# Kernel tuning notes

Hardware: AMD Instinct MI355X
Metric: run time of the kernel (lower is better)

The kernel has to match this reference:

```python
import jax, jax.numpy as jnp
import numpy as np

B, IMG, D, HEADS, L, PC, PF, OUT = 8, 128, 128, 4, 2, 8, 4, 32
HC = IMG // PC; NC = HC * HC          # 16x16 -> 256 coarse tokens
HF = IMG // PF; NF = HF * HF          # 32x32 -> 1024 fine tokens


def _ln(x, g, b):
    m = x.mean(-1, keepdims=True)
    v = x.var(-1, keepdims=True)
    return (x - m) * jax.lax.rsqrt(v + 1e-5) * g + b


def _conv(x, w, b, pad):
    y = jax.lax.conv_general_dilated(x, w, (1, 1), ((pad, pad), (pad, pad)),
                                     dimension_numbers=('NCHW', 'OIHW', 'NCHW'))
    return y + b[None, :, None, None]


def _bilinear_ac(x, oh, ow):  # F.interpolate(mode='bilinear', align_corners=True)
    _, _, H, W = x.shape
    ys = jnp.linspace(0.0, H - 1.0, oh)
    xs = jnp.linspace(0.0, W - 1.0, ow)
    y0 = jnp.floor(ys).astype(jnp.int32); y1 = jnp.minimum(y0 + 1, H - 1); wy = (ys - y0)[:, None]
    x0 = jnp.floor(xs).astype(jnp.int32); x1 = jnp.minimum(x0 + 1, W - 1); wx = (xs - x0)[None, :]
    g = lambda yi, xi: x[:, :, yi][:, :, :, xi]
    return (g(y0, x0) * (1 - wy) * (1 - wx) + g(y0, x1) * (1 - wy) * wx
            + g(y1, x0) * wy * (1 - wx) + g(y1, x1) * wy * wx)


def _patchify(x, p):  # F.unfold with kernel=stride=p, in_chans=1
    b, _, h, w = x.shape
    return x.reshape(b, h // p, p, w // p, p).transpose(0, 1, 3, 2, 4).reshape(b, (h // p) * (w // p), p * p)


def _forward(x, Wpc, bpc, Wpf, bpf, type_embed, ln1_g, ln1_b, Wqkv, Wo, bo,
             ln2_g, ln2_b, W1, b1, W2, b2, dWc, dbc, dWf, dbf, fW1, fb1, fW2, fb2):
    Bx = x.shape[0]
    # ---- multi-scale patch embed ----
    coarse = _patchify(x, PC) @ Wpc + bpc + type_embed[0]   # [B,NC,D]
    fine = _patchify(x, PF) @ Wpf + bpf                     # [B,NF,D]
    # ---- edge map: sobel -> avgpool(4) -> threshold at per-image mean ----
    gray = x.mean(1, keepdims=True)
    kx = jnp.array([[[[-1, 0, 1], [-2, 0, 2], [-1, 0, 1]]]], x.dtype)
    ky = jnp.array([[[[-1, -2, -1], [0, 0, 0], [1, 2, 1]]]], x.dtype)
    sx = _conv(gray, kx, jnp.zeros((1,), x.dtype), 1)
    sy = _conv(gray, ky, jnp.zeros((1,), x.dtype), 1)
    e = jnp.sqrt(sx ** 2 + sy ** 2)
    e = e.reshape(Bx, 1, IMG // 4, 4, IMG // 4, 4).mean((3, 5))  # [B,1,32,32] == fine grid
    mask_flat = (e > e.mean((2, 3), keepdims=True)).reshape(Bx, NF)
    # ---- static-shape analogue of per-sample masked gather + pad_sequence:
    # stable sort puts edge tokens first (original pixel order preserved), pads are zeros
    order = jnp.argsort(jnp.logical_not(mask_flat), axis=1, stable=True)   # [B,NF]
    mask_sorted = jnp.take_along_axis(mask_flat, order, 1)
    fine_sorted = jnp.take_along_axis(fine, order[..., None], 1) * mask_sorted[..., None]
    fine_sorted = fine_sorted + type_embed[1]   # type embed added to pads too (as in torch)
    tokens = jnp.concatenate([coarse, fine_sorted], axis=1)   # [B,N,D]
    N = NC + NF
    hd = D // HEADS
    scale = hd ** -0.5
    # ---- encoder blocks (pre-LN attn + MLP, irregular-token path) ----
    for l in range(L):
        y = _ln(tokens, ln1_g[l], ln1_b[l])
        qkv = (y @ Wqkv[l]).reshape(Bx, N, 3, HEADS, hd).transpose(2, 0, 3, 1, 4)
        q, k, v = qkv[0], qkv[1], qkv[2]
        attn = jax.nn.softmax(jnp.einsum('bhqd,bhkd->bhqk', q, k) * scale, axis=-1)
        o = jnp.einsum('bhqk,bhkd->bhqd', attn, v).transpose(0, 2, 1, 3).reshape(Bx, N, D)
        tokens = tokens + o @ Wo[l] + bo[l]
        y = _ln(tokens, ln2_g[l], ln2_b[l])
        tokens = tokens + jax.nn.gelu(y @ W1[l] + b1[l], approximate=False) @ W2[l] + b2[l]
    # ---- multi-scale decoder ----
    c = (tokens[:, :NC] @ dWc + dbc).reshape(Bx, HC, HC, 1).transpose(0, 3, 1, 2)
    c_up = _bilinear_ac(c, OUT, OUT)
    feats = (tokens[:, NC:] @ dWf + dbf) * mask_sorted[..., None]   # pads stay zero
    inv = jnp.argsort(order, axis=1)                                # scatter back to pixel order
    f_flat = jnp.take_along_axis(feats, inv[..., None], 1)          # [B,NF,1]
    f_map = f_flat.reshape(Bx, HF, HF, 1).transpose(0, 3, 1, 2)
    f_up = _bilinear_ac(f_map, OUT, OUT)
    fused = jnp.concatenate([c_up, f_up], axis=1)
    h = jax.nn.relu(_conv(fused, fW1, fb1, 1))
    return _conv(h, fW2, fb2, 1)   # [B,1,32,32]


def setup_inputs() -> dict:
    key = jax.random.key(0)
    ks = jax.random.split(key, 16)
    n = lambda k, shape: jax.random.normal(k, shape, jnp.float32) * 0.02
    z = lambda *shape: jnp.zeros(shape, jnp.float32)
    return {
        'x': jax.random.normal(ks[0], (B, 1, IMG, IMG), jnp.float32),
        'Wpc': n(ks[1], (PC * PC, D)), 'bpc': z(D),
        'Wpf': n(ks[2], (PF * PF, D)), 'bpf': z(D),
        'type_embed': n(ks[3], (2, D)),
        'ln1_g': jnp.ones((L, D), jnp.float32), 'ln1_b': z(L, D),
        'Wqkv': n(ks[4], (L, D, 3 * D)),
        'Wo': n(ks[5], (L, D, D)), 'bo': z(L, D),
        'ln2_g': jnp.ones((L, D), jnp.float32), 'ln2_b': z(L, D),
        'W1': n(ks[6], (L, D, 2 * D)), 'b1': z(L, 2 * D),
        'W2': n(ks[7], (L, 2 * D, D)), 'b2': z(L, D),
        'dWc': n(ks[8], (D, 1)), 'dbc': z(1),
        'dWf': n(ks[9], (D, 1)), 'dbf': z(1),
        'fW1': n(ks[10], (2, 2, 3, 3)) * 10.0, 'fb1': z(2),
        'fW2': n(ks[11], (1, 2, 3, 3)) * 10.0, 'fb2': z(1),
    }


def reference(x, Wpc, bpc, Wpf, bpf, type_embed, ln1_g, ln1_b, Wqkv, Wo, bo,
              ln2_g, ln2_b, W1, b1, W2, b2, dWc, dbc, dWf, dbf, fW1, fb1, fW2, fb2):
    return _forward(x, Wpc, bpc, Wpf, bpf, type_embed, ln1_g, ln1_b, Wqkv, Wo, bo,
                    ln2_g, ln2_b, W1, b1, W2, b2, dWc, dbc, dWf, dbf, fW1, fb1, fW2, fb2)
```

## Files before the change

kernel.cpp:

```cpp
#include <hip/hip_runtime.h>
#include <math.h>

#define Bx 8
#define IMG 128
#define DD 128
#define HEADS 4
#define LL 2
#define PCc 8
#define PFf 4
#define HCc 16
#define NCc 256
#define HFf 32
#define NFf 1024
#define NTOK 1280
#define HD 32
#define SPLIT 4
#define NQT 20

typedef __attribute__((ext_vector_type(8))) short short8;
typedef __attribute__((ext_vector_type(4))) float f32x4;

__device__ __forceinline__ short f2bf(float f) {
  unsigned u = __builtin_bit_cast(unsigned, f);
  u += 0x7FFF + ((u >> 16) & 1);
  return (short)(u >> 16);
}
__device__ __forceinline__ float bf2f(short s) {
  unsigned u = ((unsigned)(unsigned short)s) << 16;
  return __builtin_bit_cast(float, u);
}

__global__ __launch_bounds__(256) void k_prologue(const float* __restrict__ x,
    const float* __restrict__ Wpc, const float* __restrict__ bpc,
    const float* __restrict__ Wpf, const float* __restrict__ bpf,
    const float* __restrict__ te,
    const float* __restrict__ Wqkv, const float* __restrict__ Wo,
    const float* __restrict__ W1, const float* __restrict__ W2,
    short* __restrict__ WtQKV, short* __restrict__ WtO,
    short* __restrict__ Wt1, short* __restrict__ Wt2,
    float* __restrict__ e, float* __restrict__ tokens,
    float* __restrict__ fineb) {
  int blk = blockIdx.x;
  int t = threadIdx.x;
  if (blk < 1024) {
    int idx = blk * 256 + t;
    int l = idx / 131072, r = idx % 131072;
    const float* src; short* dst; int N, off;
    if (r < 49152)      { src = Wqkv + l * 49152; dst = WtQKV + l * 49152; N = 384; off = r; }
    else if (r < 65536) { src = Wo + l * 16384;  dst = WtO + l * 16384;  N = 128; off = r - 49152; }
    else if (r < 98304) { src = W1 + l * 32768;  dst = Wt1 + l * 32768;  N = 256; off = r - 65536; }
    else                { src = W2 + l * 32768;  dst = Wt2 + l * 32768;  N = 128; off = r - 98304; }
    int k = off / N, n = off % N;
    int K = (r >= 98304) ? 256 : 128;
    dst[(size_t)n * K + k] = f2bf(src[off]);
  } else if (blk < 1536) {
    int bt = blk - 1024;
    int b = bt >> 6, tile = bt & 63;
    int ty = tile >> 3, tx = tile & 7;
    int ly = t >> 4, lx = t & 15;
    int py = ty * 16 + ly, px = tx * 16 + lx;
    const float* img = x + (size_t)b * IMG * IMG;
    float v[3][3];
    #pragma unroll
    for (int ky = 0; ky < 3; ++ky)
      #pragma unroll
      for (int kx = 0; kx < 3; ++kx) {
        int yy = py + ky - 1, xx = px + kx - 1;
        v[ky][kx] = (yy >= 0 && yy < IMG && xx >= 0 && xx < IMG)
                        ? img[yy * IMG + xx] : 0.f;
      }
    float gx = -v[0][0] + v[0][2] - 2.f * v[1][0] + 2.f * v[1][2] - v[2][0] + v[2][2];
    float gy = -v[0][0] - 2.f * v[0][1] - v[0][2] + v[2][0] + 2.f * v[2][1] + v[2][2];
    __shared__ float sm[256];
    sm[t] = sqrtf(gx * gx + gy * gy);
    __syncthreads();
    if (t < 16) {
      int cy = t >> 2, cx = t & 3;
      float s = 0.f;
      #pragma unroll
      for (int dy = 0; dy < 4; ++dy)
        #pragma unroll
        for (int dx = 0; dx < 4; ++dx) s += sm[(cy * 4 + dy) * 16 + cx * 4 + dx];
      e[b * NFf + (ty * 4 + cy) * 32 + tx * 4 + cx] = s * (1.f / 16.f);
    }
  } else if (blk < 2560) {
    int bt = (blk - 1536) * 2 + (t >> 7);
    int b = bt / NCc, tok = bt % NCc;
    int hc = tok / HCc, wc = tok % HCc;
    int half = t >> 7, d = t & 127;
    __shared__ float patch[2][PCc * PCc];
    if (d < PCc * PCc) {
      int pi = d / PCc, pj = d % PCc;
      patch[half][d] = x[(b * IMG + hc * PCc + pi) * IMG + wc * PCc + pj];
    }
    __syncthreads();
    float acc = bpc[d] + te[d];
    #pragma unroll 8
    for (int i = 0; i < PCc * PCc; ++i) acc += patch[half][i] * Wpc[i * DD + d];
    tokens[(size_t)(b * NTOK + tok) * DD + d] = acc;
  } else {
    int ft = (blk - 2560) * 2 + (t >> 7);
    int b = ft >> 10, tloc = ft & 1023;
    int hf = tloc >> 5, wf = tloc & 31;
    int half = t >> 7, d = t & 127;
    __shared__ float patch[2][PFf * PFf];
    if (d < PFf * PFf) {
      int pi = d / PFf, pj = d % PFf;
      patch[half][d] = x[(b * IMG + hf * PFf + pi) * IMG + wf * PFf + pj];
    }
    __syncthreads();
    float acc = bpf[d];
    #pragma unroll
    for (int i = 0; i < PFf * PFf; ++i) acc += patch[half][i] * Wpf[i * DD + d];
    fineb[(size_t)(b * NFf + tloc) * DD + d] = acc;
  }
}

__global__ __launch_bounds__(1024) void k_edge_sort(const float* __restrict__ e,
    int* __restrict__ order, float* __restrict__ msort) {
  int b = blockIdx.x;
  int t = threadIdx.x;
  int lane = t & 63, wave = t >> 6;
  float ev = e[b * NFf + t];
  __shared__ float wsum[16];
  __shared__ int wcnt[16];
  float r = ev;
  #pragma unroll
  for (int o = 32; o > 0; o >>= 1) r += __shfl_xor(r, o, 64);
  if (lane == 0) wsum[wave] = r;
  __syncthreads();
  float tot = 0.f;
  #pragma unroll
  for (int i = 0; i < 16; ++i) tot += wsum[i];
  float mean = tot * (1.f / 1024.f);
  int m = (ev > mean) ? 1 : 0;
  unsigned long long bal = __ballot(m);
  if (lane == 0) wcnt[wave] = __popcll(bal);
  __syncthreads();
  int wbase = 0, total = 0;
  #pragma unroll
  for (int i = 0; i < 16; ++i) {
    int c = wcnt[i];
    if (i < wave) wbase += c;
    total += c;
  }
  unsigned long long below = (lane == 63) ? ~0ULL : ((1ULL << (lane + 1)) - 1);
  int incl = __popcll(bal & below);
  int eb = wbase + incl - m;
  int pos = m ? eb : (total + t - eb);
  order[b * NFf + pos] = t;
  msort[b * NFf + pos] = (float)m;
}

__global__ __launch_bounds__(256) void k_gather_ln(float* __restrict__ tokens,
    const float* __restrict__ fineb, const int* __restrict__ order,
    const float* __restrict__ msort, const float* __restrict__ te,
    const float* __restrict__ g, const float* __restrict__ bb,
    short* __restrict__ outp) {
  int row = blockIdx.x * 4 + (threadIdx.x >> 6);
  int lane = threadIdx.x & 63;
  int b = row / NTOK, r = row % NTOK;
  float2 v;
  if (r < NCc) {
    v = ((const float2*)(tokens + (size_t)row * DD))[lane];
  } else {
    int pos = r - NCc;
    int src = order[b * NFf + pos];
    float mk = msort[b * NFf + pos];
    float2 u = ((const float2*)(fineb + (size_t)(b * NFf + src) * DD))[lane];
    float2 tv = ((const float2*)(te + DD))[lane];
    v.x = u.x * mk + tv.x;
    v.y = u.y * mk + tv.y;
    ((float2*)(tokens + (size_t)row * DD))[lane] = v;
  }
  float s = v.x + v.y;
  #pragma unroll
  for (int o = 32; o > 0; o >>= 1) s += __shfl_xor(s, o, 64);
  float mean = s * (1.f / 128.f);
  float cx = v.x - mean, cy = v.y - mean;
  float q = cx * cx + cy * cy;
  #pragma unroll
  for (int o = 32; o > 0; o >>= 1) q += __shfl_xor(q, o, 64);
  float rstd = rsqrtf(q * (1.f / 128.f) + 1e-5f);
  float2 gg = ((const float2*)g)[lane];
  float2 bv = ((const float2*)bb)[lane];
  int p = (int)(unsigned short)f2bf(cx * rstd * gg.x + bv.x)
        | ((int)(unsigned short)f2bf(cy * rstd * gg.y + bv.y) << 16);
  ((int*)(outp + (size_t)row * DD))[lane] = p;
}

__global__ __launch_bounds__(256) void k_gemm_mfma(const short* __restrict__ A,
    const short* __restrict__ Wt, const float* __restrict__ bias,
    float* __restrict__ Cf, short* __restrict__ Cb, int K, int N, int do_gelu) {
  __shared__ short Alds[64 * 128];
  __shared__ short Blds[64 * 128];
  int row0 = blockIdx.x * 64, col0 = blockIdx.y * 64;
  int t = threadIdx.x;
  int lane = t & 63, w = t >> 6;
  int m = lane & 15, quad = lane >> 4;
  int lrow = lane >> 4, jphys = lane & 15;
  f32x4 zero = {0.f, 0.f, 0.f, 0.f};
  f32x4 acc[4] = {zero, zero, zero, zero};

  for (int kb = 0; kb < K; kb += 128) {
    __syncthreads();
    #pragma unroll
    for (int j = 0; j < 4; ++j) {
      int c = j * 4 + w;
      int r = c * 4 + lrow;
      int jlog = jphys ^ (r & 15);
      __builtin_amdgcn_global_load_lds(
          (const unsigned*)&A[(size_t)(row0 + r) * K + kb + jlog * 8],
          (unsigned*)&Alds[c * 512], 16, 0, 0);
      __builtin_amdgcn_global_load_lds(
          (const unsigned*)&Wt[(size_t)(col0 + r) * K + kb + jlog * 8],
          (unsigned*)&Blds[c * 512], 16, 0, 0);
    }
    __syncthreads();
    #pragma unroll
    for (int ks = 0; ks < 4; ++ks) {
      int pc = ((quad + ks * 4) ^ m) * 8;
      short8 af = *(const short8*)&Alds[(w * 16 + m) * 128 + pc];
      #pragma unroll
      for (int nt = 0; nt < 4; ++nt) {
        short8 bf = *(const short8*)&Blds[(nt * 16 + m) * 128 + pc];
        acc[nt] = __builtin_amdgcn_mfma_f32_16x16x32_bf16(af, bf, acc[nt], 0, 0, 0);
      }
    }
  }
  #pragma unroll
  for (int nt = 0; nt < 4; ++nt) {
    int col = col0 + nt * 16 + m;
    float bv = bias ? bias[col] : 0.f;
    #pragma unroll
    for (int r = 0; r < 4; ++r) {
      int row = row0 + w * 16 + quad * 4 + r;
      float v = acc[nt][r] + bv;
      if (do_gelu) v = 0.5f * v * (1.f + erff(v * 0.70710678118654752f));
      if (Cf) Cf[(size_t)row * N + col] += v;
      else    Cb[(size_t)row * N + col] = f2bf(v);
    }
  }
}

__global__ __launch_bounds__(256) void k_fused(const short* __restrict__ Opart,
    const float* __restrict__ Lpart, const short* __restrict__ WtO,
    const float* __restrict__ bo_, const float* __restrict__ ln2g_,
    const float* __restrict__ ln2b_, const short* __restrict__ Wt1,
    const float* __restrict__ b1_, const short* __restrict__ Wt2,
    const float* __restrict__ b2_, float* __restrict__ tokens,
    const float* __restrict__ ln1g_, const float* __restrict__ ln1b_,
    const short* __restrict__ WtQ, short* __restrict__ qkvb) {
  __shared__ short Blds[128 * 128];
  __shared__ short AH[32 * 268];
  __shared__ short Ylds[32 * 136];
  __shared__ float pls[2][32], plq[2][32];
  int row0 = blockIdx.x * 32;
  int b = row0 / NTOK;
  int rloc = row0 % NTOK;
  int qt = rloc >> 6, qoff = rloc & 63;
  int t = threadIdx.x;
  int lane = t & 63, w = t >> 6;
  int m = lane & 15, quad = lane >> 4;
  int rt = w >> 1, ch = w & 1;
  int lrow = lane >> 4, jphys = lane & 15;
  f32x4 zero = {0.f, 0.f, 0.f, 0.f};

  #pragma unroll
  for (int j = 0; j < 8; ++j) {
    int c = j * 4 + w;
    int r = c * 4 + lrow;
    int jlog = jphys ^ (r & 15);
    __builtin_amdgcn_global_load_lds(
        (const unsigned*)&WtO[(size_t)r * 128 + jlog * 8],
        (unsigned*)&Blds[c * 512], 16, 0, 0);
  }
  #pragma unroll
  for (int it = 0; it < 2; ++it) {
    int idx = t + it * 256;
    int q = idx >> 4, j = idx & 15;
    int dh = j >> 2, dd = (j & 3) * 8;
    int qg = qoff + q;
    size_t pb = ((size_t)(b * HEADS + dh) * NQT + qt) * SPLIT;
    float L = Lpart[(pb + 0) * 64 + qg] + Lpart[(pb + 1) * 64 + qg]
            + Lpart[(pb + 2) * 64 + qg] + Lpart[(pb + 3) * 64 + qg];
    float o[8] = {0, 0, 0, 0, 0, 0, 0, 0};
    #pragma unroll
    for (int sk = 0; sk < SPLIT; ++sk) {
      short8 po = *(const short8*)&Opart[(pb + sk) * 2048 + qg * 32 + dd];
      #pragma unroll
      for (int i = 0; i < 8; ++i) o[i] += bf2f(po[i]);
    }
    float rs = 1.f / L;
    short8 ov;
    #pragma unroll
    for (int i = 0; i < 8; ++i) ov[i] = f2bf(o[i] * rs);
    *(short8*)&AH[q * 136 + j * 8] = ov;
  }
  __syncthreads();
  f32x4 acc[4] = {zero, zero, zero, zero};
  #pragma unroll
  for (int ks = 0; ks < 4; ++ks) {
    short8 af = *(const short8*)&AH[(rt * 16 + m) * 136 + quad * 8 + ks * 32];
    int pc = ((quad + ks * 4) ^ m) * 8;
    #pragma unroll
    for (int nt = 0; nt < 4; ++nt) {
      short8 bf = *(const short8*)&Blds[(ch * 64 + nt * 16 + m) * 128 + pc];
      acc[nt] = __builtin_amdgcn_mfma_f32_16x16x32_bf16(af, bf, acc[nt], 0, 0, 0);
    }
  }
  float v[4][4];
  #pragma unroll
  for (int nt = 0; nt < 4; ++nt) {
    int col = ch * 64 + nt * 16 + m;
    float bv = bo_[col];
    #pragma unroll
    for (int r = 0; r < 4; ++r) {
      int row = row0 + rt * 16 + quad * 4 + r;
      v[nt][r] = acc[nt][r] + bv + tokens[(size_t)row * DD + col];
    }
  }
  #pragma unroll
  for (int r = 0; r < 4; ++r) {
    float s = v[0][r] + v[1][r] + v[2][r] + v[3][r];
    float q = v[0][r] * v[0][r] + v[1][r] * v[1][r]
            + v[2][r] * v[2][r] + v[3][r] * v[3][r];
    #pragma unroll
    for (int o = 1; o < 16; o <<= 1) { s += __shfl_xor(s, o); q += __shfl_xor(q, o); }
    if (m == 0) {
      int lr = rt * 16 + quad * 4 + r;
      pls[ch][lr] = s;
      plq[ch][lr] = q;
    }
  }
  __syncthreads();
  #pragma unroll
  for (int r = 0; r < 4; ++r) {
    int lr = rt * 16 + quad * 4 + r;
    float S = pls[0][lr] + pls[1][lr];
    float Q = plq[0][lr] + plq[1][lr];
    float mean = S * (1.f / 128.f);
    float var = Q * (1.f / 128.f) - mean * mean;
    float rstd = rsqrtf(var + 1e-5f);
    #pragma unroll
    for (int nt = 0; nt < 4; ++nt) {
      int col = ch * 64 + nt * 16 + m;
      Ylds[lr * 136 + col] = f2bf((v[nt][r] - mean) * rstd * ln2g_[col] + ln2b_[col]);
    }
  }
  for (int hh = 0; hh < 2; ++hh) {
    #pragma unroll
    for (int j = 0; j < 8; ++j) {
      int c = j * 4 + w;
      int r = c * 4 + lrow;
      int jlog = jphys ^ (r & 15);
      __builtin_amdgcn_global_load_lds(
          (const unsigned*)&Wt1[(size_t)(hh * 128 + r) * 128 + jlog * 8],
          (unsigned*)&Blds[c * 512], 16, 0, 0);
    }
    __syncthreads();
    f32x4 ha[4] = {zero, zero, zero, zero};
    #pragma unroll
    for (int ks = 0; ks < 4; ++ks) {
      short8 af = *(const short8*)&Ylds[(rt * 16 + m) * 136 + quad * 8 + ks * 32];
      int pc = ((quad + ks * 4) ^ m) * 8;
      #pragma unroll
      for (int nt = 0; nt < 4; ++nt) {
        short8 bf = *(const short8*)&Blds[(ch * 64 + nt * 16 + m) * 128 + pc];
        ha[nt] = __builtin_amdgcn_mfma_f32_16x16x32_bf16(af, bf, ha[nt], 0, 0, 0);
      }
    }
    #pragma unroll
    for (int nt = 0; nt < 4; ++nt) {
      int n = hh * 128 + ch * 64 + nt * 16 + m;
      float bv = b1_[n];
      #pragma unroll
      for (int r = 0; r < 4; ++r) {
        float vv = ha[nt][r] + bv;
        vv = 0.5f * vv * (1.f + erff(vv * 0.70710678118654752f));
        AH[(rt * 16 + quad * 4 + r) * 268 + n] = f2bf(vv);
      }
    }
    __syncthreads();
  }
  f32x4 a2[4] = {zero, zero, zero, zero};
  for (int kb = 0; kb < 2; ++kb) {
    if (kb) __syncthreads();
    #pragma unroll
    for (int j = 0; j < 8; ++j) {
      int c = j * 4 + w;
      int r = c * 4 + lrow;
      int jlog = jphys ^ (r & 15);
      __builtin_amdgcn_global_load_lds(
          (const unsigned*)&Wt2[(size_t)r * 256 + kb * 128 + jlog * 8],
          (unsigned*)&Blds[c * 512], 16, 0, 0);
    }
    __syncthreads();
    #pragma unroll
    for (int ks = 0; ks < 4; ++ks) {
      int pc = ((quad + ks * 4) ^ m) * 8;
      short8 af = *(const short8*)&AH[(rt * 16 + m) * 268 + kb * 128
                                      + quad * 8 + ks * 32];
      #pragma unroll
      for (int nt = 0; nt < 4; ++nt) {
        short8 bf = *(const short8*)&Blds[(ch * 64 + nt * 16 + m) * 128 + pc];
        a2[nt] = __builtin_amdgcn_mfma_f32_16x16x32_bf16(af, bf, a2[nt], 0, 0, 0);
      }
    }
  }
  #pragma unroll
  for (int nt = 0; nt < 4; ++nt) {
    int col = ch * 64 + nt * 16 + m;
    float bv = b2_[col];
    #pragma unroll
    for (int r = 0; r < 4; ++r) {
      int row = row0 + rt * 16 + quad * 4 + r;
      float val = a2[nt][r] + bv + v[nt][r];
      tokens[(size_t)row * DD + col] = val;
      v[nt][r] = val;
    }
  }
  if (ln1g_ == nullptr) return;
  #pragma unroll
  for (int r = 0; r < 4; ++r) {
    float s = v[0][r] + v[1][r] + v[2][r] + v[3][r];
    float q = v[0][r] * v[0][r] + v[1][r] * v[1][r]
            + v[2][r] * v[2][r] + v[3][r] * v[3][r];
    #pragma unroll
    for (int o = 1; o < 16; o <<= 1) { s += __shfl_xor(s, o); q += __shfl_xor(q, o); }
    if (m == 0) {
      int lr = rt * 16 + quad * 4 + r;
      pls[ch][lr] = s;
      plq[ch][lr] = q;
    }
  }
  __syncthreads();
  #pragma unroll
  for (int r = 0; r < 4; ++r) {
    int lr = rt * 16 + quad * 4 + r;
    float S = pls[0][lr] + pls[1][lr];
    float Q = plq[0][lr] + plq[1][lr];
    float mean = S * (1.f / 128.f);
    float var = Q * (1.f / 128.f) - mean * mean;
    float rstd = rsqrtf(var + 1e-5f);
    #pragma unroll
    for (int nt = 0; nt < 4; ++nt) {
      int col = ch * 64 + nt * 16 + m;
      Ylds[lr * 136 + col] = f2bf((v[nt][r] - mean) * rstd * ln1g_[col] + ln1b_[col]);
    }
  }
  for (int c3 = 0; c3 < 3; ++c3) {
    if (c3) __syncthreads();
    #pragma unroll
    for (int j = 0; j < 8; ++j) {
      int c = j * 4 + w;
      int r = c * 4 + lrow;
      int jlog = jphys ^ (r & 15);
      __builtin_amdgcn_global_load_lds(
          (const unsigned*)&WtQ[(size_t)(c3 * 128 + r) * 128 + jlog * 8],
          (unsigned*)&Blds[c * 512], 16, 0, 0);
    }
    __syncthreads();
    f32x4 qa[4] = {zero, zero, zero, zero};
    #pragma unroll
    for (int ks = 0; ks < 4; ++ks) {
      short8 af = *(const short8*)&Ylds[(rt * 16 + m) * 136 + quad * 8 + ks * 32];
      int pc = ((quad + ks * 4) ^ m) * 8;
      #pragma unroll
      for (int nt = 0; nt < 4; ++nt) {
        short8 bf = *(const short8*)&Blds[(ch * 64 + nt * 16 + m) * 128 + pc];
        qa[nt] = __builtin_amdgcn_mfma_f32_16x16x32_bf16(af, bf, qa[nt], 0, 0, 0);
      }
    }
    #pragma unroll
    for (int nt = 0; nt < 4; ++nt) {
      int col = c3 * 128 + ch * 64 + nt * 16 + m;
      #pragma unroll
      for (int r = 0; r < 4; ++r) {
        int row = row0 + rt * 16 + quad * 4 + r;
        qkvb[(size_t)row * 384 + col] = f2bf(qa[nt][r]);
      }
    }
  }
}

__global__ __launch_bounds__(256) void k_attn4(const short* __restrict__ qkv,
    short* __restrict__ Opart, float* __restrict__ Lpart) {
  __shared__ short Ks[64 * 32];
  __shared__ short Vt[32 * 74];
  __shared__ short Pl[4][16 * 74];

  int sk = blockIdx.x % SPLIT;
  int qt = (blockIdx.x / SPLIT) % NQT;
  int h  = (blockIdx.x / (SPLIT * NQT)) % HEADS;
  int b  = blockIdx.x / (SPLIT * NQT * HEADS);
  int t = threadIdx.x;
  int lane = t & 63, w = t >> 6;
  int m = lane & 15, quad = lane >> 4;
  int q0 = qt * 64 + w * 16;

  const float scale = 0.17677669529663687f;
  short8 qraw = *(const short8*)(qkv + ((size_t)(b * NTOK) + q0 + m) * 384 + h * HD + quad * 8);
  short8 qf;
  #pragma unroll
  for (int j = 0; j < 8; ++j) qf[j] = f2bf(bf2f(qraw[j]) * scale);

  f32x4 zero = {0.f, 0.f, 0.f, 0.f};
  f32x4 Oacc[2] = {zero, zero};
  float psum[4] = {0.f, 0.f, 0.f, 0.f};

  int skey = t >> 2, sdseg = t & 3;
  int jlogK = sdseg ^ ((skey >> 1) & 3);
  const short* kstage = qkv + ((size_t)(b * NTOK) + skey) * 384 + 128 + h * HD + jlogK * 8;
  const short* vstage = qkv + ((size_t)(b * NTOK) + skey) * 384 + 256 + h * HD + sdseg * 8;
  int kswz = (quad ^ ((m >> 1) & 3)) * 8;

  for (int s = sk * 5; s < sk * 5 + 5; ++s) {
    __syncthreads();
    __builtin_amdgcn_global_load_lds((const unsigned*)(kstage + (size_t)s * 64 * 384),
                                     (unsigned*)&Ks[w * 512], 16, 0, 0);
    short8 vf = *(const short8*)(vstage + (size_t)s * 64 * 384);
    #pragma unroll
    for (int j = 0; j < 8; ++j) Vt[(sdseg * 8 + j) * 74 + skey] = vf[j];
    __syncthreads();

    f32x4 sc[4];
    #pragma unroll
    for (int ct = 0; ct < 4; ++ct) {
      short8 kfrag = *(const short8*)&Ks[(ct * 16 + m) * 32 + kswz];
      sc[ct] = __builtin_amdgcn_mfma_f32_16x16x32_bf16(qf, kfrag, zero, 0, 0, 0);
    }
    #pragma unroll
    for (int ct = 0; ct < 4; ++ct)
      #pragma unroll
      for (int r = 0; r < 4; ++r) {
        float p = __expf(sc[ct][r]);
        unsigned u = __builtin_bit_cast(unsigned, p);
        psum[r] += __builtin_bit_cast(float, u & 0xffff0000u);
        Pl[w][(quad * 4 + r) * 74 + ct * 16 + m] = (short)(u >> 16);
      }
    #pragma unroll
    for (int ks = 0; ks < 2; ++ks) {
      short8 pfrag = *(const short8*)&Pl[w][m * 74 + ks * 32 + quad * 8];
      #pragma unroll
      for (int nt = 0; nt < 2; ++nt) {
        short8 vfrag = *(const short8*)&Vt[(nt * 16 + m) * 74 + ks * 32 + quad * 8];
        Oacc[nt] = __builtin_amdgcn_mfma_f32_16x16x32_bf16(pfrag, vfrag, Oacc[nt], 0, 0, 0);
      }
    }
  }
  #pragma unroll
  for (int r = 0; r < 4; ++r) {
    float ssum = psum[r];
    #pragma unroll
    for (int o = 1; o < 16; o <<= 1) ssum += __shfl_xor(ssum, o);
    int qloc = w * 16 + quad * 4 + r;
    #pragma unroll
    for (int nt = 0; nt < 2; ++nt)
      Opart[(size_t)blockIdx.x * 2048 + qloc * 32 + nt * 16 + m] = f2bf(Oacc[nt][r]);
    if (m == 0) Lpart[(size_t)blockIdx.x * 64 + qloc] = ssum;
  }
}

__global__ __launch_bounds__(1024) void k_decoder(const float* __restrict__ tokens,
    const float* __restrict__ dWc, const float* __restrict__ dbc,
    const float* __restrict__ dWf, const float* __restrict__ dbf,
    const float* __restrict__ msort, const int* __restrict__ order,
    const float* __restrict__ fW1, const float* __restrict__ fb1,
    const float* __restrict__ fW2, const float* __restrict__ fb2,
    float* __restrict__ outp) {
  int b = blockIdx.x;
  int t = threadIdx.x;
  __shared__ float cmap[NCc];
  __shared__ float fmap[1024];
  __shared__ float cup[1024];
  __shared__ float hb[2][1024];
  {
    const float* row = tokens + (size_t)(b * NTOK + NCc + t) * DD;
    float a = 0.f;
    #pragma unroll 8
    for (int d4 = 0; d4 < 32; ++d4) {
      float4 u = ((const float4*)row)[d4];
      float4 wv = ((const float4*)dWf)[d4];
      a += u.x * wv.x + u.y * wv.y + u.z * wv.z + u.w * wv.w;
    }
    a = (a + dbf[0]) * msort[b * NFf + t];
    fmap[order[b * NFf + t]] = a;
  }
  if (t < NCc) {
    const float* row = tokens + (size_t)(b * NTOK + t) * DD;
    float a = 0.f;
    #pragma unroll 8
    for (int d4 = 0; d4 < 32; ++d4) {
      float4 u = ((const float4*)row)[d4];
      float4 wv = ((const float4*)dWc)[d4];
      a += u.x * wv.x + u.y * wv.y + u.z * wv.z + u.w * wv.w;
    }
    cmap[t] = a + dbc[0];
  }
  __syncthreads();
  int y = t >> 5, x = t & 31;
  {
    float ys = y * (15.f / 31.f);
    float xs = x * (15.f / 31.f);
    int y0 = (int)floorf(ys); int y1 = min(y0 + 1, 15); float wy = ys - (float)y0;
    int x0 = (int)floorf(xs); int x1 = min(x0 + 1, 15); float wx = xs - (float)x0;
    cup[t] = cmap[y0 * 16 + x0] * (1.f - wy) * (1.f - wx)
           + cmap[y0 * 16 + x1] * (1.f - wy) * wx
           + cmap[y1 * 16 + x0] * wy * (1.f - wx)
           + cmap[y1 * 16 + x1] * wy * wx;
  }
  __syncthreads();
  for (int oc = 0; oc < 2; ++oc) {
    float a = fb1[oc];
    #pragma unroll
    for (int ic = 0; ic < 2; ++ic)
      #pragma unroll
      for (int ky = 0; ky < 3; ++ky)
        #pragma unroll
        for (int kx = 0; kx < 3; ++kx) {
          int yy = y + ky - 1, xx = x + kx - 1;
          float v = 0.f;
          if (yy >= 0 && yy < 32 && xx >= 0 && xx < 32)
            v = ic == 0 ? cup[yy * 32 + xx] : fmap[yy * 32 + xx];
          a += v * fW1[((oc * 2 + ic) * 3 + ky) * 3 + kx];
        }
    hb[oc][t] = fmaxf(a, 0.f);
  }
  __syncthreads();
  float a = fb2[0];
  #pragma unroll
  for (int ic = 0; ic < 2; ++ic)
    #pragma unroll
    for (int ky = 0; ky < 3; ++ky)
      #pragma unroll
      for (int kx = 0; kx < 3; ++kx) {
        int yy = y + ky - 1, xx = x + kx - 1;
        float v = (yy >= 0 && yy < 32 && xx >= 0 && xx < 32)
                      ? hb[ic][yy * 32 + xx] : 0.f;
        a += v * fW2[(ic * 3 + ky) * 3 + kx];
      }
  outp[b * 1024 + t] = a;
}

extern "C" void kernel_launch(void* const* d_in, const int* in_sizes, int n_in,
                              void* d_out, int out_size, void* d_ws, size_t ws_size,
                              hipStream_t stream) {
  const float* x    = (const float*)d_in[0];
  const float* Wpc  = (const float*)d_in[1];
  const float* bpc  = (const float*)d_in[2];
  const float* Wpf  = (const float*)d_in[3];
  const float* bpf  = (const float*)d_in[4];
  const float* te   = (const float*)d_in[5];
  const float* ln1g = (const float*)d_in[6];
  const float* ln1b = (const float*)d_in[7];
  const float* Wqkv = (const float*)d_in[8];
  const float* Wo   = (const float*)d_in[9];
  const float* bo   = (const float*)d_in[10];
  const float* ln2g = (const float*)d_in[11];
  const float* ln2b = (const float*)d_in[12];
  const float* W1   = (const float*)d_in[13];
  const float* b1   = (const float*)d_in[14];
  const float* W2   = (const float*)d_in[15];
  const float* b2   = (const float*)d_in[16];
  const float* dWc  = (const float*)d_in[17];
  const float* dbc  = (const float*)d_in[18];
  const float* dWf  = (const float*)d_in[19];
  const float* dbf  = (const float*)d_in[20];
  const float* fW1  = (const float*)d_in[21];
  const float* fb1  = (const float*)d_in[22];
  const float* fW2  = (const float*)d_in[23];
  const float* fb2  = (const float*)d_in[24];

  char* ws = (char*)d_ws;
  float* tokens = (float*)ws;                 ws += 1310720 * 4;
  float* fineb  = (float*)ws;                 ws += 1048576 * 4;
  short* ybuf   = (short*)ws;                 ws += 1310720 * 2;
  short* qkvb   = (short*)ws;                 ws += 3932160 * 2;
  short* Opart  = (short*)ws;                 ws += (size_t)(Bx * HEADS * NQT * SPLIT) * 2048 * 2;
  float* Lpart  = (float*)ws;                 ws += (size_t)(Bx * HEADS * NQT * SPLIT) * 64 * 4;
  short* WtQKV  = (short*)ws;                 ws += 98304 * 2;
  short* WtO    = (short*)ws;                 ws += 32768 * 2;
  short* Wt1    = (short*)ws;                 ws += 65536 * 2;
  short* Wt2    = (short*)ws;                 ws += 65536 * 2;
  float* ebuf   = (float*)ws;                 ws += 8192 * 4;
  float* msort  = (float*)ws;                 ws += 8192 * 4;
  int*   order  = (int*)ws;                   ws += 8192 * 4;

  const int M = Bx * NTOK;

  k_prologue<<<6656, 256, 0, stream>>>(x, Wpc, bpc, Wpf, bpf, te, Wqkv, Wo, W1, W2,
                                       WtQKV, WtO, Wt1, Wt2, ebuf, tokens, fineb);
  k_edge_sort<<<Bx, 1024, 0, stream>>>(ebuf, order, msort);
  k_gather_ln<<<M / 4, 256, 0, stream>>>(tokens, fineb, order, msort, te,
                                         ln1g, ln1b, ybuf);

  k_gemm_mfma<<<dim3(M / 64, 384 / 64), 256, 0, stream>>>(
      ybuf, WtQKV, nullptr, nullptr, qkvb, 128, 384, 0);
  k_attn4<<<Bx * HEADS * NQT * SPLIT, 256, 0, stream>>>(qkvb, Opart, Lpart);
  k_fused<<<M / 32, 256, 0, stream>>>(
      Opart, Lpart, WtO, bo, ln2g, ln2b,
      Wt1, b1, Wt2, b2, tokens,
      ln1g + DD, ln1b + DD, WtQKV + 49152, qkvb);

  k_attn4<<<Bx * HEADS * NQT * SPLIT, 256, 0, stream>>>(qkvb, Opart, Lpart);
  k_fused<<<M / 32, 256, 0, stream>>>(
      Opart, Lpart, WtO + 16384, bo + DD, ln2g + DD, ln2b + DD,
      Wt1 + 32768, b1 + 256, Wt2 + 32768, b2 + DD, tokens,
      nullptr, nullptr, nullptr, nullptr);

  k_decoder<<<Bx, 1024, 0, stream>>>(tokens, dWc, dbc, dWf, dbf, msort, order,
                                     fW1, fb1, fW2, fb2, (float*)d_out);
}
```

Measured before the change: 236.1 us.

## Fuse gather+LN1 with QKV GEMM and move decoder projection into last fused kernel

Merges the gather/LayerNorm kernel and the separate QKV GEMM into a single kernel that normalizes 32 rows into LDS and multiplies them by the QKV weight. This removes the bf16 ybuf round trip and one launch. The final fused layer now computes the per-token decoder dot products (dWc/dWf) from registers and writes a small hrow buffer, so the decoder no longer rereads the full token tensor. It also issues weight tile loads earlier so they overlap the LayerNorm math. The trade-off is extra sync points and larger LDS use in the gather kernel.

```diff
diff --git a/kernel.cpp b/kernel.cpp
--- a/kernel.cpp
+++ b/kernel.cpp
@@ -152,93 +152,96 @@
   msort[b * NFf + pos] = (float)m;
 }
 
-__global__ __launch_bounds__(256) void k_gather_ln(float* __restrict__ tokens,
+__global__ __launch_bounds__(256) void k_gather_qkv(float* __restrict__ tokens,
     const float* __restrict__ fineb, const int* __restrict__ order,
     const float* __restrict__ msort, const float* __restrict__ te,
     const float* __restrict__ g, const float* __restrict__ bb,
-    short* __restrict__ outp) {
-  int row = blockIdx.x * 4 + (threadIdx.x >> 6);
-  int lane = threadIdx.x & 63;
-  int b = row / NTOK, r = row % NTOK;
-  float2 v;
-  if (r < NCc) {
-    v = ((const float2*)(tokens + (size_t)row * DD))[lane];
-  } else {
-    int pos = r - NCc;
-    int src = order[b * NFf + pos];
-    float mk = msort[b * NFf + pos];
-    float2 u = ((const float2*)(fineb + (size_t)(b * NFf + src) * DD))[lane];
-    float2 tv = ((const float2*)(te + DD))[lane];
-    v.x = u.x * mk + tv.x;
-    v.y = u.y * mk + tv.y;
-    ((float2*)(tokens + (size_t)row * DD))[lane] = v;
-  }
-  float s = v.x + v.y;
-  #pragma unroll
-  for (int o = 32; o > 0; o >>= 1) s += __shfl_xor(s, o, 64);
-  float mean = s * (1.f / 128.f);
-  float cx = v.x - mean, cy = v.y - mean;
-  float q = cx * cx + cy * cy;
-  #pragma unroll
-  for (int o = 32; o > 0; o >>= 1) q += __shfl_xor(q, o, 64);
-  float rstd = rsqrtf(q * (1.f / 128.f) + 1e-5f);
-  float2 gg = ((const float2*)g)[lane];
-  float2 bv = ((const float2*)bb)[lane];
-  int p = (int)(unsigned short)f2bf(cx * rstd * gg.x + bv.x)
-        | ((int)(unsigned short)f2bf(cy * rstd * gg.y + bv.y) << 16);
-  ((int*)(outp + (size_t)row * DD))[lane] = p;
-}
-
-__global__ __launch_bounds__(256) void k_gemm_mfma(const short* __restrict__ A,
-    const short* __restrict__ Wt, const float* __restrict__ bias,
-    float* __restrict__ Cf, short* __restrict__ Cb, int K, int N, int do_gelu) {
-  __shared__ short Alds[64 * 128];
-  __shared__ short Blds[64 * 128];
-  int row0 = blockIdx.x * 64, col0 = blockIdx.y * 64;
+    const short* __restrict__ WtQ, short* __restrict__ qkvb) {
+  __shared__ short Blds[128 * 128];
+  __shared__ short Ylds[32 * 136];
+  int row0 = blockIdx.x * 32;
   int t = threadIdx.x;
   int lane = t & 63, w = t >> 6;
   int m = lane & 15, quad = lane >> 4;
+  int rt = w >> 1, ch = w & 1;
   int lrow = lane >> 4, jphys = lane & 15;
   f32x4 zero = {0.f, 0.f, 0.f, 0.f};
-  f32x4 acc[4] = {zero, zero, zero, zero};
-
-  for (int kb = 0; kb < K; kb += 128) {
-    __syncthreads();
-    #pragma unroll
-    for (int j = 0; j < 4; ++j) {
-      int c = j * 4 + w;
-      int r = c * 4 + lrow;
-      int jlog = jphys ^ (r & 15);
-      __builtin_amdgcn_global_load_lds(
-          (const unsigned*)&A[(size_t)(row0 + r) * K + kb + jlog * 8],
-          (unsigned*)&Alds[c * 512], 16, 0, 0);
-      __builtin_amdgcn_global_load_lds(
-          (const unsigned*)&Wt[(size_t)(col0 + r) * K + kb + jlog * 8],
-          (unsigned*)&Blds[c * 512], 16, 0, 0);
-    }
-    __syncthreads();
+
+  #pragma unroll
+  for (int j = 0; j < 8; ++j) {
+    int c = j * 4 + w;
+    int r = c * 4 + lrow;
+    int jlog = jphys ^ (r & 15);
+    __builtin_amdgcn_global_load_lds(
+        (const unsigned*)&WtQ[(size_t)r * 128 + jlog * 8],
+        (unsigned*)&Blds[c * 512], 16, 0, 0);
+  }
+  float2 gg = ((const float2*)g)[lane];
+  float2 bv = ((const float2*)bb)[lane];
+  #pragma unroll
+  for (int rr = 0; rr < 8; ++rr) {
+    int lr = w * 8 + rr;
+    int row = row0 + lr;
+    int b = row / NTOK, rl = row % NTOK;
+    float2 v;
+    if (rl < NCc) {
+      v = ((const float2*)(tokens + (size_t)row * DD))[lane];
+    } else {
+      int pos = rl - NCc;
+      int src = order[b * NFf + pos];
+      float mk = msort[b * NFf + pos];
+      float2 u = ((const float2*)(fineb + (size_t)(b * NFf + src) * DD))[lane];
+      float2 tv = ((const float2*)(te + DD))[lane];
+      v.x = u.x * mk + tv.x;
+      v.y = u.y * mk + tv.y;
+      ((float2*)(tokens + (size_t)row * DD))[lane] = v;
+    }
+    float s = v.x + v.y;
+    #pragma unroll
+    for (int o = 32; o > 0; o >>= 1) s += __shfl_xor(s, o, 64);
+    float mean = s * (1.f / 128.f);
+    float cx = v.x - mean, cy = v.y - mean;
+    float q = cx * cx + cy * cy;
+    #pragma unroll
+    for (int o = 32; o > 0; o >>= 1) q += __shfl_xor(q, o, 64);
+    float rstd = rsqrtf(q * (1.f / 128.f) + 1e-5f);
+    int p = (int)(unsigned short)f2bf(cx * rstd * gg.x + bv.x)
+          | ((int)(unsigned short)f2bf(cy * rstd * gg.y + bv.y) << 16);
+    ((int*)Ylds)[lr * 68 + lane] = p;
+  }
+  for (int c3 = 0; c3 < 3; ++c3) {
+    if (c3) {
+      __syncthreads();
+      #pragma unroll
+      for (int j = 0; j < 8; ++j) {
+        int c = j * 4 + w;
+        int r = c * 4 + lrow;
+        int jlog = jphys ^ (r & 15);
+        __builtin_amdgcn_global_load_lds(
+            (const unsigned*)&WtQ[(size_t)(c3 * 128 + r) * 128 + jlog * 8],
+            (unsigned*)&Blds[c * 512], 16, 0, 0);
+      }
+    }
+    __syncthreads();
+    f32x4 qa[4] = {zero, zero, zero, zero};
     #pragma unroll
     for (int ks = 0; ks < 4; ++ks) {
+      short8 af = *(const short8*)&Ylds[(rt * 16 + m) * 136 + quad * 8 + ks * 32];
       int pc = ((quad + ks * 4) ^ m) * 8;
-      short8 af = *(const short8*)&Alds[(w * 16 + m) * 128 + pc];
       #pragma unroll
       for (int nt = 0; nt < 4; ++nt) {
-        short8 bf = *(const short8*)&Blds[(nt * 16 + m) * 128 + pc];
-        acc[nt] = __builtin_amdgcn_mfma_f32_16x16x32_bf16(af, bf, acc[nt], 0, 0, 0);
-      }
-    }
-  }
-  #pragma unroll
-  for (int nt = 0; nt < 4; ++nt) {
-    int col = col0 + nt * 16 + m;
-    float bv = bias ? bias[col] : 0.f;
-    #pragma unroll
-    for (int r = 0; r < 4; ++r) {
-      int row = row0 + w * 16 + quad * 4 + r;
-      float v = acc[nt][r] + bv;
-      if (do_gelu) v = 0.5f * v * (1.f + erff(v * 0.70710678118654752f));
-      if (Cf) Cf[(size_t)row * N + col] += v;
-      else    Cb[(size_t)row * N + col] = f2bf(v);
+        short8 bf = *(const short8*)&Blds[(ch * 64 + nt * 16 + m) * 128 + pc];
+        qa[nt] = __builtin_amdgcn_mfma_f32_16x16x32_bf16(af, bf, qa[nt], 0, 0, 0);
+      }
+    }
+    #pragma unroll
+    for (int nt = 0; nt < 4; ++nt) {
+      int col = c3 * 128 + ch * 64 + nt * 16 + m;
+      #pragma unroll
+      for (int r = 0; r < 4; ++r) {
+        int row = row0 + rt * 16 + quad * 4 + r;
+        qkvb[(size_t)row * 384 + col] = f2bf(qa[nt][r]);
+      }
     }
   }
 }
@@ -250,7 +253,10 @@
     const float* __restrict__ b1_, const short* __restrict__ Wt2,
     const float* __restrict__ b2_, float* __restrict__ tokens,
     const float* __restrict__ ln1g_, const float* __restrict__ ln1b_,
-    const short* __restrict__ WtQ, short* __restrict__ qkvb) {
+    const short* __restrict__ WtQ, short* __restrict__ qkvb,
+    const float* __restrict__ dWc_, const float* __restrict__ dbc_,
+    const float* __restrict__ dWf_, const float* __restrict__ dbf_,
+    float* __restrict__ hrow) {
   __shared__ short Blds[128 * 128];
   __shared__ short AH[32 * 268];
   __shared__ short Ylds[32 * 136];
@@ -335,6 +341,15 @@
   }
   __syncthreads();
   #pragma unroll
+  for (int j = 0; j < 8; ++j) {
+    int c = j * 4 + w;
+    int r = c * 4 + lrow;
+    int jlog = jphys ^ (r & 15);
+    __builtin_amdgcn_global_load_lds(
+        (const unsigned*)&Wt1[(size_t)r * 128 + jlog * 8],
+        (unsigned*)&Blds[c * 512], 16, 0, 0);
+  }
+  #pragma unroll
   for (int r = 0; r < 4; ++r) {
     int lr = rt * 16 + quad * 4 + r;
     float S = pls[0][lr] + pls[1][lr];
@@ -349,14 +364,17 @@
     }
   }
   for (int hh = 0; hh < 2; ++hh) {
-    #pragma unroll
-    for (int j = 0; j < 8; ++j) {
-      int c = j * 4 + w;
-      int r = c * 4 + lrow;
-      int jlog = jphys ^ (r & 15);
-      __builtin_amdgcn_global_load_lds(
-          (const unsigned*)&Wt1[(size_t)(hh * 128 + r) * 128 + jlog * 8],
-          (unsigned*)&Blds[c * 512], 16, 0, 0);
+    if (hh) {
+      __syncthreads();
+      #pragma unroll
+      for (int j = 0; j < 8; ++j) {
+        int c = j * 4 + w;
+        int r = c * 4 + lrow;
+        int jlog = jphys ^ (r & 15);
+        __builtin_amdgcn_global_load_lds(
+            (const unsigned*)&Wt1[(size_t)(128 + r) * 128 + jlog * 8],
+            (unsigned*)&Blds[c * 512], 16, 0, 0);
+      }
     }
     __syncthreads();
     f32x4 ha[4] = {zero, zero, zero, zero};
@@ -381,11 +399,10 @@
         AH[(rt * 16 + quad * 4 + r) * 268 + n] = f2bf(vv);
       }
     }
-    __syncthreads();
   }
   f32x4 a2[4] = {zero, zero, zero, zero};
   for (int kb = 0; kb < 2; ++kb) {
-    if (kb) __syncthreads();
+    __syncthreads();
     #pragma unroll
     for (int j = 0; j < 8; ++j) {
       int c = j * 4 + w;
@@ -420,7 +437,31 @@
       v[nt][r] = val;
     }
   }
-  if (ln1g_ == nullptr) return;
+  if (ln1g_ == nullptr) {
+    bool coarse = (rloc < NCc);
+    const float* dw = coarse ? dWc_ : dWf_;
+    float dwv[4];
+    #pragma unroll
+    for (int nt = 0; nt < 4; ++nt) dwv[nt] = dw[ch * 64 + nt * 16 + m];
+    #pragma unroll
+    for (int r = 0; r < 4; ++r) {
+      float s = v[0][r] * dwv[0] + v[1][r] * dwv[1]
+              + v[2][r] * dwv[2] + v[3][r] * dwv[3];
+      #pragma unroll
+      for (int o = 1; o < 16; o <<= 1) s += __shfl_xor(s, o);
+      if (m == 0) pls[ch][rt * 16 + quad * 4 + r] = s;
+    }
+    __syncthreads();
+    if (m == 0 && ch == 0) {
+      float dbv = coarse ? dbc_[0] : dbf_[0];
+      #pragma unroll
+      for (int r = 0; r < 4; ++r) {
+        int lr = rt * 16 + quad * 4 + r;
+        hrow[row0 + lr] = pls[0][lr] + pls[1][lr] + dbv;
+      }
+    }
+    return;
+  }
   #pragma unroll
   for (int r = 0; r < 4; ++r) {
     float s = v[0][r] + v[1][r] + v[2][r] + v[3][r];
@@ -435,6 +476,15 @@
     }
   }
   __syncthreads();
+  #pragma unroll
+  for (int j = 0; j < 8; ++j) {
+    int c = j * 4 + w;
+    int r = c * 4 + lrow;
+    int jlog = jphys ^ (r & 15);
+    __builtin_amdgcn_global_load_lds(
+        (const unsigned*)&WtQ[(size_t)r * 128 + jlog * 8],
+        (unsigned*)&Blds[c * 512], 16, 0, 0);
+  }
   #pragma unroll
   for (int r = 0; r < 4; ++r) {
     int lr = rt * 16 + quad * 4 + r;
@@ -450,15 +500,17 @@
     }
   }
   for (int c3 = 0; c3 < 3; ++c3) {
-    if (c3) __syncthreads();
-    #pragma unroll
-    for (int j = 0; j < 8; ++j) {
-      int c = j * 4 + w;
-      int r = c * 4 + lrow;
-      int jlog = jphys ^ (r & 15);
-      __builtin_amdgcn_global_load_lds(
-          (const unsigned*)&WtQ[(size_t)(c3 * 128 + r) * 128 + jlog * 8],
-          (unsigned*)&Blds[c * 512], 16, 0, 0);
+    if (c3) {
+      __syncthreads();
+      #pragma unroll
+      for (int j = 0; j < 8; ++j) {
+        int c = j * 4 + w;
+        int r = c * 4 + lrow;
+        int jlog = jphys ^ (r & 15);
+        __builtin_amdgcn_global_load_lds(
+            (const unsigned*)&WtQ[(size_t)(c3 * 128 + r) * 128 + jlog * 8],
+            (unsigned*)&Blds[c * 512], 16, 0, 0);
+      }
     }
     __syncthreads();
     f32x4 qa[4] = {zero, zero, zero, zero};
@@ -562,9 +614,7 @@
   }
 }
 
-__global__ __launch_bounds__(1024) void k_decoder(const float* __restrict__ tokens,
-    const float* __restrict__ dWc, const float* __restrict__ dbc,
-    const float* __restrict__ dWf, const float* __restrict__ dbf,
+__global__ __launch_bounds__(1024) void k_decoder(const float* __restrict__ hrow,
     const float* __restrict__ msort, const int* __restrict__ order,
     const float* __restrict__ fW1, const float* __restrict__ fb1,
     const float* __restrict__ fW2, const float* __restrict__ fb2,
@@ -575,29 +625,8 @@
   __shared__ float fmap[1024];
   __shared__ float cup[1024];
   __shared__ float hb[2][1024];
-  {
-    const float* row = tokens + (size_t)(b * NTOK + NCc + t) * DD;
-    float a = 0.f;
-    #pragma unroll 8
-    for (int d4 = 0; d4 < 32; ++d4) {
-      float4 u = ((const float4*)row)[d4];
-      float4 wv = ((const float4*)dWf)[d4];
-      a += u.x * wv.x + u.y * wv.y + u.z * wv.z + u.w * wv.w;
-    }
-    a = (a + dbf[0]) * msort[b * NFf + t];
-    fmap[order[b * NFf + t]] = a;
-  }
-  if (t < NCc) {
-    const float* row = tokens + (size_t)(b * NTOK + t) * DD;
-    float a = 0.f;
-    #pragma unroll 8
-    for (int d4 = 0; d4 < 32; ++d4) {
-      float4 u = ((const float4*)row)[d4];
-      float4 wv = ((const float4*)dWc)[d4];
-      a += u.x * wv.x + u.y * wv.y + u.z * wv.z + u.w * wv.w;
-    }
-    cmap[t] = a + dbc[0];
-  }
+  fmap[order[b * NFf + t]] = hrow[b * NTOK + NCc + t] * msort[b * NFf + t];
+  if (t < NCc) cmap[t] = hrow[b * NTOK + t];
   __syncthreads();
   int y = t >> 5, x = t & 31;
   {
@@ -675,7 +704,6 @@
   char* ws = (char*)d_ws;
   float* tokens = (float*)ws;                 ws += 1310720 * 4;
   float* fineb  = (float*)ws;                 ws += 1048576 * 4;
-  short* ybuf   = (short*)ws;                 ws += 1310720 * 2;
   short* qkvb   = (short*)ws;                 ws += 3932160 * 2;
   short* Opart  = (short*)ws;                 ws += (size_t)(Bx * HEADS * NQT * SPLIT) * 2048 * 2;
   float* Lpart  = (float*)ws;                 ws += (size_t)(Bx * HEADS * NQT * SPLIT) * 64 * 4;
@@ -686,29 +714,30 @@
   float* ebuf   = (float*)ws;                 ws += 8192 * 4;
   float* msort  = (float*)ws;                 ws += 8192 * 4;
   int*   order  = (int*)ws;                   ws += 8192 * 4;
+  float* hrow   = (float*)ws;                 ws += 10240 * 4;
 
   const int M = Bx * NTOK;
 
   k_prologue<<<6656, 256, 0, stream>>>(x, Wpc, bpc, Wpf, bpf, te, Wqkv, Wo, W1, W2,
                                        WtQKV, WtO, Wt1, Wt2, ebuf, tokens, fineb);
   k_edge_sort<<<Bx, 1024, 0, stream>>>(ebuf, order, msort);
-  k_gather_ln<<<M / 4, 256, 0, stream>>>(tokens, fineb, order, msort, te,
-                                         ln1g, ln1b, ybuf);
-
-  k_gemm_mfma<<<dim3(M / 64, 384 / 64), 256, 0, stream>>>(
-      ybuf, WtQKV, nullptr, nullptr, qkvb, 128, 384, 0);
+  k_gather_qkv<<<M / 32, 256, 0, stream>>>(tokens, fineb, order, msort, te,
+                                           ln1g, ln1b, WtQKV, qkvb);
+
   k_attn4<<<Bx * HEADS * NQT * SPLIT, 256, 0, stream>>>(qkvb, Opart, Lpart);
   k_fused<<<M / 32, 256, 0, stream>>>(
       Opart, Lpart, WtO, bo, ln2g, ln2b,
       Wt1, b1, Wt2, b2, tokens,
-      ln1g + DD, ln1b + DD, WtQKV + 49152, qkvb);
+      ln1g + DD, ln1b + DD, WtQKV + 49152, qkvb,
+      nullptr, nullptr, nullptr, nullptr, nullptr);
 
   k_attn4<<<Bx * HEADS * NQT * SPLIT, 256, 0, stream>>>(qkvb, Opart, Lpart);
   k_fused<<<M / 32, 256, 0, stream>>>(
       Opart, Lpart, WtO + 16384, bo + DD, ln2g + DD, ln2b + DD,
       Wt1 + 32768, b1 + 256, Wt2 + 32768, b2 + DD, tokens,
-      nullptr, nullptr, nullptr, nullptr);
-
-  k_decoder<<<Bx, 1024, 0, stream>>>(tokens, dWc, dbc, dWf, dbf, msort, order,
+      nullptr, nullptr, nullptr, nullptr,
+      dWc, dbc, dWf, dbf, hrow);
+
+  k_decoder<<<Bx, 1024, 0, stream>>>(hrow, msort, order,
                                      fW1, fb1, fW2, fb2, (float*)d_out);
 }
```

Result: faster. 228.4 us (-3.3%).
